# Optimization experiments

Measured on AMD Instinct MI355X. Metric: run time of the kernel, lower is better.

The kernel has to match this reference:

```python
import jax, jax.numpy as jnp
import numpy as np

HEADS = 16
HEAD_DIM = 64  # hidden_dim // heads = 1024 // 16


def setup_inputs() -> dict:
    key = jax.random.key(0)
    ks = jax.random.split(key, 7)
    B, S, D = 2, 2048, 1024
    x = jax.random.normal(ks[0], (B, S, D), dtype=jnp.float32)
    mask = jax.random.randint(ks[1], (B, 1, S, S), 0, 2, dtype=jnp.int32)
    scale = 1.0 / np.sqrt(D)
    Wq = jax.random.normal(ks[2], (D, D), dtype=jnp.float32) * scale
    Wk = jax.random.normal(ks[3], (D, D), dtype=jnp.float32) * scale
    Wv = jax.random.normal(ks[4], (D, D), dtype=jnp.float32) * scale
    Wo = jax.random.normal(ks[5], (D, D), dtype=jnp.float32) * scale
    bo = jnp.zeros((D,), dtype=jnp.float32)
    return {"x": x, "mask": mask, "Wq": Wq, "Wk": Wk, "Wv": Wv, "Wo": Wo, "bo": bo}


def _split_heads(t):
    # (B, S, D) -> (B, H, S, Hd)
    B, S, D = t.shape
    return t.reshape(B, S, HEADS, HEAD_DIM).transpose(0, 2, 1, 3)


def reference(x, mask, Wq, Wk, Wv, Wo, bo):
    B, S, D = x.shape
    # torch nn.Linear: y = x @ W.T (weights stored [out, in])
    q = _split_heads(x @ Wq.T)
    k = _split_heads(x @ Wk.T)
    v = _split_heads(x @ Wv.T)
    scores = jnp.einsum("bhqd,bhkd->bhqk", q, k) / jnp.sqrt(jnp.float32(HEAD_DIM))
    scores = jnp.where(mask == 1, jnp.float32(-1e9), scores)
    attn = jax.nn.softmax(scores, axis=-1)
    # dropout p=0.0 (eval) -> identity
    out = jnp.einsum("bhqk,bhkd->bhqd", attn, v)
    out = out.transpose(0, 2, 1, 3).reshape(B, S, D)
    return out @ Wo.T + bo
```

## Files before the change

kernel.cpp:

```cpp
#include <hip/hip_runtime.h>
#include <hip/hip_bf16.h>

typedef __attribute__((ext_vector_type(4))) float f32x4;
typedef __attribute__((ext_vector_type(8))) short bf16x8;

#define MFMA16(a, b, c) __builtin_amdgcn_mfma_f32_16x16x32_bf16(a, b, c, 0, 0, 0)

#define AS1(p) ((const __attribute__((address_space(1))) void*)(p))
#define AS3(p) ((__attribute__((address_space(3))) void*)(p))

#define SWZ(r) ((((r) & 7)) ^ ((((r) >> 3) & 1) << 2))

__device__ __forceinline__ unsigned short f2bf(float f) {
  union { float f; unsigned u; } x; x.f = f;
  unsigned r = x.u + 0x7fffu + ((x.u >> 16) & 1u);
  return (unsigned short)(r >> 16);
}

__global__ __launch_bounds__(256) void convert_all(
    const float* __restrict__ x, const float* __restrict__ wq,
    const float* __restrict__ wk, const float* __restrict__ wv,
    const float* __restrict__ wo, unsigned short* __restrict__ dst) {
  const int NX = 4194304, NW = 1048576, TOT = NX + 4 * NW;
  for (int i = blockIdx.x * 256 + threadIdx.x; i < TOT; i += gridDim.x * 256) {
    float v;
    if (i < NX) {
      v = x[i];
    } else {
      int j = i - NX; int ws = j >> 20; int o = j & (NW - 1);
      v = (ws == 0) ? wq[o] : (ws == 1) ? wk[o] : (ws == 2) ? wv[o] : wo[o];
    }
    dst[i] = f2bf(v);
  }
}

__global__ __launch_bounds__(256) void convert_mask(
    const int* __restrict__ m, unsigned char* __restrict__ o) {
  const int i = blockIdx.x * 256 + threadIdx.x;
  const int4 v = ((const int4*)m)[i];
  uchar4 r;
  r.x = (unsigned char)v.x; r.y = (unsigned char)v.y;
  r.z = (unsigned char)v.z; r.w = (unsigned char)v.w;
  ((uchar4*)o)[i] = r;
}

__device__ __forceinline__ void gemm_nt_128(
    const unsigned short* __restrict__ A, const unsigned short* __restrict__ Bw,
    int m0, int n0, unsigned short* Al, unsigned short* Bl, f32x4 acc[4][4]) {
  const int t = threadIdx.x;
  const int l = t & 63;
  const int w = t >> 6, wr = w >> 1, wc = w & 1;
  const int lc = l & 15, lg = l >> 4;

  auto stage = [&](int buf, int kt) {
    const int k0 = kt * 32;
#pragma unroll
    for (int c = 0; c < 2; ++c) {
      const int e = (t + c * 256) * 8;
      const int row = e >> 5, col = e & 31;
      __builtin_amdgcn_global_load_lds(
          AS1(A + (size_t)(m0 + row) * 1024 + k0 + col),
          AS3(Al + buf * 4096 + (w * 64 + c * 256) * 8), 16, 0, 0);
      __builtin_amdgcn_global_load_lds(
          AS1(Bw + (size_t)(n0 + row) * 1024 + k0 + col),
          AS3(Bl + buf * 4096 + (w * 64 + c * 256) * 8), 16, 0, 0);
    }
  };

  stage(0, 0);
#pragma unroll 2
  for (int kt = 0; kt < 32; ++kt) {
    __syncthreads();
    if (kt + 1 < 32) stage((kt + 1) & 1, kt + 1);
    const unsigned short* Ab = Al + (kt & 1) * 4096;
    const unsigned short* Bb = Bl + (kt & 1) * 4096;
    bf16x8 af[4], bfr[4];
#pragma unroll
    for (int i = 0; i < 4; ++i)
      af[i] = *(const bf16x8*)(Ab + (wr * 64 + i * 16 + lc) * 32 + lg * 8);
#pragma unroll
    for (int j = 0; j < 4; ++j)
      bfr[j] = *(const bf16x8*)(Bb + (wc * 64 + j * 16 + lc) * 32 + lg * 8);
#pragma unroll
    for (int i = 0; i < 4; ++i)
#pragma unroll
      for (int j = 0; j < 4; ++j)
        acc[i][j] = MFMA16(af[i], bfr[j], acc[i][j]);
  }
}

__global__ __launch_bounds__(256) void gemm_qkv(
    const unsigned short* __restrict__ xb,
    const unsigned short* __restrict__ wqb, const unsigned short* __restrict__ wkb,
    const unsigned short* __restrict__ wvb,
    unsigned short* __restrict__ q, unsigned short* __restrict__ k,
    unsigned short* __restrict__ vt) {
  __shared__ unsigned short Al[2 * 4096], Bl[2 * 4096];
  const int z = blockIdx.z;
  const unsigned short* Bw = (z == 0) ? wqb : (z == 1) ? wkb : wvb;
  const int m0 = blockIdx.x * 128, n0 = blockIdx.y * 128;
  f32x4 acc[4][4] = {};
  gemm_nt_128(xb, Bw, m0, n0, Al, Bl, acc);

  const int l = threadIdx.x & 63, w = threadIdx.x >> 6;
  const int wr = w >> 1, wc = w & 1, lc = l & 15, lg = l >> 4;

  if (z == 2) {
#pragma unroll
    for (int i = 0; i < 4; ++i)
#pragma unroll
      for (int j = 0; j < 4; ++j) {
        const int m = m0 + wr * 64 + i * 16 + lg * 4;
        const int n = n0 + wc * 64 + j * 16 + lc;
        const int b = m >> 11, s = m & 2047, hh = n >> 6, hd = n & 63;
        ushort4 pk;
        pk.x = f2bf(acc[i][j][0]); pk.y = f2bf(acc[i][j][1]);
        pk.z = f2bf(acc[i][j][2]); pk.w = f2bf(acc[i][j][3]);
        *(ushort4*)(vt + (size_t)((b << 4) + hh) * 131072 + (size_t)hd * 2048 + s) = pk;
      }
  } else {
    unsigned short* C = (z == 0) ? q : k;
#pragma unroll
    for (int i = 0; i < 4; ++i)
#pragma unroll
      for (int j = 0; j < 4; ++j)
#pragma unroll
        for (int r = 0; r < 4; ++r) {
          const int m = m0 + wr * 64 + i * 16 + lg * 4 + r;
          const int n = n0 + wc * 64 + j * 16 + lc;
          const int b = m >> 11, s = m & 2047, hh = n >> 6, hd = n & 63;
          C[(size_t)((b << 4) + hh) * 131072 + s * 64 + hd] = f2bf(acc[i][j][r]);
        }
  }
}

__global__ __launch_bounds__(256) void gemm_out(
    const unsigned short* __restrict__ ao, const unsigned short* __restrict__ wob,
    const float* __restrict__ bias, float* __restrict__ out) {
  __shared__ unsigned short Al[2 * 4096], Bl[2 * 4096];
  const int m0 = blockIdx.x * 128, n0 = blockIdx.y * 128;
  f32x4 acc[4][4] = {};
  gemm_nt_128(ao, wob, m0, n0, Al, Bl, acc);

  const int l = threadIdx.x & 63, w = threadIdx.x >> 6;
  const int wr = w >> 1, wc = w & 1, lc = l & 15, lg = l >> 4;
#pragma unroll
  for (int i = 0; i < 4; ++i)
#pragma unroll
    for (int j = 0; j < 4; ++j)
#pragma unroll
      for (int r = 0; r < 4; ++r) {
        const int m = m0 + wr * 64 + i * 16 + lg * 4 + r;
        const int n = n0 + wc * 64 + j * 16 + lc;
        out[(size_t)m * 1024 + n] = acc[i][j][r] + bias[n];
      }
}

__global__ __launch_bounds__(256, 4) void attn_fwd(
    const unsigned short* __restrict__ q, const unsigned short* __restrict__ k,
    const unsigned short* __restrict__ vt, const unsigned char* __restrict__ mb8,
    unsigned short* __restrict__ ao) {
  __shared__ unsigned short Kl[2][4096];
  __shared__ unsigned short Vl[2][4096];
  __shared__ unsigned short Pl[4][1024];
  const int bh = blockIdx.y, b = bh >> 4;
  const int q0 = blockIdx.x * 64;
  const int t = threadIdx.x, l = t & 63, w = t >> 6;
  const int lc = l & 15, lg = l >> 4;

  const unsigned short* qp = q + ((size_t)bh * 2048 + q0 + w * 16) * 64;
  bf16x8 qa[2];
  qa[0] = *(const bf16x8*)(qp + lc * 64 + lg * 8);
  qa[1] = *(const bf16x8*)(qp + lc * 64 + 32 + lg * 8);

  bf16x8 onesf;
#pragma unroll
  for (int j = 0; j < 8; ++j) ((unsigned short*)&onesf)[j] = (lc == 0) ? 0x3F80 : 0;

  const unsigned short* kp = k + (size_t)bh * 131072;
  const unsigned short* vp = vt + (size_t)bh * 131072;
  const unsigned char* mp = mb8 + (size_t)b * 4194304 + (size_t)(q0 + w * 16 + lg * 4) * 2048;

  f32x4 oa[4] = {};
  f32x4 lsum = {};

  auto stage = [&](int buf, int kv0) {
#pragma unroll
    for (int c = 0; c < 2; ++c) {
      const int ldc = (c * 4 + w) * 64 + l;
      const int row = ldc >> 3, ch = ldc & 7;
      const int sch = ch ^ SWZ(row);
      __builtin_amdgcn_global_load_lds(
          AS1(kp + (size_t)(kv0 + row) * 64 + sch * 8),
          AS3(&Kl[buf][(c * 4 + w) * 512]), 16, 0, 0);
      __builtin_amdgcn_global_load_lds(
          AS1(vp + (size_t)row * 2048 + kv0 + sch * 8),
          AS3(&Vl[buf][(c * 4 + w) * 512]), 16, 0, 0);
    }
  };

  stage(0, 0);
  for (int tt = 0; tt < 32; ++tt) {
    const int kv0 = tt * 64;
    __syncthreads();
    if (tt + 1 < 32) stage((tt + 1) & 1, kv0 + 64);
    const unsigned short* Kb = Kl[tt & 1];
    const unsigned short* Vb = Vl[tt & 1];

    f32x4 sa[4];
#pragma unroll
    for (int cb = 0; cb < 4; ++cb)
#pragma unroll
      for (int r = 0; r < 4; ++r)
        sa[cb][r] = -240000.f * (float)mp[(size_t)r * 2048 + kv0 + cb * 16 + lc];

#pragma unroll
    for (int cb = 0; cb < 4; ++cb) {
      const int row = cb * 16 + lc;
#pragma unroll
      for (int h2 = 0; h2 < 2; ++h2) {
        bf16x8 kf = *(const bf16x8*)(Kb + row * 64 + ((h2 * 4 + lg) ^ SWZ(row)) * 8);
        sa[cb] = MFMA16(qa[h2], kf, sa[cb]);
      }
    }

    unsigned short* Pw = (unsigned short*)Pl[w];
#pragma unroll
    for (int cb = 0; cb < 4; ++cb)
#pragma unroll
      for (int r = 0; r < 4; ++r) {
        const float p = __expf(sa[cb][r] * 0.125f);
        const int qr = lg * 4 + r;
        const int slot = (cb * 2 + (lc >> 3)) ^ SWZ(qr);
        Pw[qr * 64 + slot * 8 + (lc & 7)] = f2bf(p);
      }

#pragma unroll
    for (int kk = 0; kk < 2; ++kk) {
      bf16x8 pa = *(const bf16x8*)(Pw + lc * 64 + ((kk * 4 + lg) ^ SWZ(lc)) * 8);
      lsum = MFMA16(pa, onesf, lsum);
#pragma unroll
      for (int db = 0; db < 4; ++db) {
        const int d = db * 16 + lc;
        bf16x8 vf = *(const bf16x8*)(Vb + d * 64 + ((kk * 4 + lg) ^ SWZ(d)) * 8);
        oa[db] = MFMA16(pa, vf, oa[db]);
      }
    }
  }

  float li[4];
#pragma unroll
  for (int r = 0; r < 4; ++r) li[r] = __shfl(lsum[r], l & 48, 64);
#pragma unroll
  for (int r = 0; r < 4; ++r) {
    const float inv = 1.0f / li[r];
    const int row = q0 + w * 16 + lg * 4 + r;
    unsigned short* dst = ao + ((size_t)b * 2048 + row) * 1024 + (bh & 15) * 64;
#pragma unroll
    for (int db = 0; db < 4; ++db) dst[db * 16 + lc] = f2bf(oa[db][r] * inv);
  }
}

extern "C" void kernel_launch(void* const* d_in, const int* in_sizes, int n_in,
                              void* d_out, int out_size, void* d_ws, size_t ws_size,
                              hipStream_t stream) {
  const float* x = (const float*)d_in[0];
  const int* mask = (const int*)d_in[1];
  const float* Wq = (const float*)d_in[2];
  const float* Wk = (const float*)d_in[3];
  const float* Wv = (const float*)d_in[4];
  const float* Wo = (const float*)d_in[5];
  const float* bo = (const float*)d_in[6];

  unsigned short* ws = (unsigned short*)d_ws;
  unsigned short* xb = ws;
  unsigned short* wqb = xb + 4194304;
  unsigned short* wkb = wqb + 1048576;
  unsigned short* wvb = wkb + 1048576;
  unsigned short* wob = wvb + 1048576;
  unsigned short* qb = wob + 1048576;
  unsigned short* kb = qb + 4194304;
  unsigned short* vtb = kb + 4194304;
  unsigned short* aob = vtb + 4194304;

  unsigned char* mb8 = (unsigned char*)xb;

  convert_all<<<dim3(4096), dim3(256), 0, stream>>>(x, Wq, Wk, Wv, Wo, ws);
  gemm_qkv<<<dim3(32, 8, 3), dim3(256), 0, stream>>>(xb, wqb, wkb, wvb, qb, kb, vtb);
  convert_mask<<<dim3(8192), dim3(256), 0, stream>>>(mask, mb8);
  attn_fwd<<<dim3(32, 32), dim3(256), 0, stream>>>(qb, kb, vtb, mb8, aob);
  gemm_out<<<dim3(32, 8), dim3(256), 0, stream>>>(aob, wob, bo, (float*)d_out);
}
```

Measured before the change: 258.8 us.

## Transpose score MFMA, vectorize mask loads and P stores, remap attention blocks

Swaps the MFMA operands so each lane holds four consecutive key columns for one query row. This lets the mask be read as one 32-bit word per lane instead of four byte loads, and lets P be written as packed 8-byte bf16 stores using hardware exp2 and paired bf16 conversion. The grid is flattened and remapped so blocks sharing a head are spread across XCD-interleaved block IDs, aiming for better L2 reuse of K/V. The risk is that the new LDS write pattern for P is less conflict-friendly, and the remap assumes an 8-way XCD layout.

```diff
diff --git a/kernel.cpp b/kernel.cpp
--- a/kernel.cpp
+++ b/kernel.cpp
@@ -163,8 +163,10 @@
   __shared__ unsigned short Kl[2][4096];
   __shared__ unsigned short Vl[2][4096];
   __shared__ unsigned short Pl[4][1024];
-  const int bh = blockIdx.y, b = bh >> 4;
-  const int q0 = blockIdx.x * 64;
+  const int orig = blockIdx.x;
+  const int nid = (orig & 7) * 128 + (orig >> 3);
+  const int bh = nid >> 5, b = bh >> 4;
+  const int q0 = (nid & 31) * 64;
   const int t = threadIdx.x, l = t & 63, w = t >> 6;
   const int lc = l & 15, lg = l >> 4;
 
@@ -179,7 +181,7 @@
 
   const unsigned short* kp = k + (size_t)bh * 131072;
   const unsigned short* vp = vt + (size_t)bh * 131072;
-  const unsigned char* mp = mb8 + (size_t)b * 4194304 + (size_t)(q0 + w * 16 + lg * 4) * 2048;
+  const unsigned char* mp = mb8 + (size_t)b * 4194304 + (size_t)(q0 + w * 16 + lc) * 2048;
 
   f32x4 oa[4] = {};
   f32x4 lsum = {};
@@ -209,10 +211,13 @@
 
     f32x4 sa[4];
 #pragma unroll
-    for (int cb = 0; cb < 4; ++cb)
-#pragma unroll
-      for (int r = 0; r < 4; ++r)
-        sa[cb][r] = -240000.f * (float)mp[(size_t)r * 2048 + kv0 + cb * 16 + lc];
+    for (int cb = 0; cb < 4; ++cb) {
+      const unsigned mw = *(const unsigned*)(mp + kv0 + cb * 16 + lg * 4);
+      sa[cb][0] = -240000.f * (float)(mw & 255u);
+      sa[cb][1] = -240000.f * (float)((mw >> 8) & 255u);
+      sa[cb][2] = -240000.f * (float)((mw >> 16) & 255u);
+      sa[cb][3] = -240000.f * (float)(mw >> 24);
+    }
 
 #pragma unroll
     for (int cb = 0; cb < 4; ++cb) {
@@ -220,20 +225,25 @@
 #pragma unroll
       for (int h2 = 0; h2 < 2; ++h2) {
         bf16x8 kf = *(const bf16x8*)(Kb + row * 64 + ((h2 * 4 + lg) ^ SWZ(row)) * 8);
-        sa[cb] = MFMA16(qa[h2], kf, sa[cb]);
+        sa[cb] = MFMA16(kf, qa[h2], sa[cb]);
       }
     }
 
     unsigned short* Pw = (unsigned short*)Pl[w];
 #pragma unroll
-    for (int cb = 0; cb < 4; ++cb)
-#pragma unroll
-      for (int r = 0; r < 4; ++r) {
-        const float p = __expf(sa[cb][r] * 0.125f);
-        const int qr = lg * 4 + r;
-        const int slot = (cb * 2 + (lc >> 3)) ^ SWZ(qr);
-        Pw[qr * 64 + slot * 8 + (lc & 7)] = f2bf(p);
-      }
+    for (int cb = 0; cb < 4; ++cb) {
+      float2 ab, cd;
+      ab.x = __builtin_amdgcn_exp2f(sa[cb][0] * 0.18033688f);
+      ab.y = __builtin_amdgcn_exp2f(sa[cb][1] * 0.18033688f);
+      cd.x = __builtin_amdgcn_exp2f(sa[cb][2] * 0.18033688f);
+      cd.y = __builtin_amdgcn_exp2f(sa[cb][3] * 0.18033688f);
+      __hip_bfloat162 lo = __float22bfloat162_rn(ab);
+      __hip_bfloat162 hi = __float22bfloat162_rn(cd);
+      uint2 pk;
+      pk.x = *(unsigned*)&lo;
+      pk.y = *(unsigned*)&hi;
+      *(uint2*)(Pw + lc * 64 + ((cb * 2 + (lg >> 1)) ^ SWZ(lc)) * 8 + (lg & 1) * 4) = pk;
+    }
 
 #pragma unroll
     for (int kk = 0; kk < 2; ++kk) {
@@ -288,6 +298,6 @@
   convert_all<<<dim3(4096), dim3(256), 0, stream>>>(x, Wq, Wk, Wv, Wo, ws);
   gemm_qkv<<<dim3(32, 8, 3), dim3(256), 0, stream>>>(xb, wqb, wkb, wvb, qb, kb, vtb);
   convert_mask<<<dim3(8192), dim3(256), 0, stream>>>(mask, mb8);
-  attn_fwd<<<dim3(32, 32), dim3(256), 0, stream>>>(qb, kb, vtb, mb8, aob);
+  attn_fwd<<<dim3(1024), dim3(256), 0, stream>>>(qb, kb, vtb, mb8, aob);
   gemm_out<<<dim3(32, 8), dim3(256), 0, stream>>>(aob, wob, bo, (float*)d_out);
 }
```

After: 269.0 us. 4.0% more time.
